# Performance work log

Measured on AMD Instinct MI355X. Metric: run time of the kernel, lower is better.

Reference implementation:

```python
import jax, jax.numpy as jnp
import numpy as np

N = 50000   # nodes
D = 128     # hidden dim
E_NS = 250000  # non-self-loop edges
B = 4096    # sessions
NEG_SLOPE = 0.01  # F.leaky_relu default


def setup_inputs() -> dict:
    key = jax.random.key(0)
    ks = jax.random.split(key, 8)
    x = jax.random.normal(ks[0], (N, D), jnp.float32)
    src = jax.random.randint(ks[1], (E_NS,), 0, N)
    off = jax.random.randint(ks[2], (E_NS,), 1, N)
    dst = (src + off) % N  # guarantees src != dst
    loops = jnp.arange(N)
    edge_index = jnp.stack([jnp.concatenate([src, loops]),
                            jnp.concatenate([dst, loops])])  # [2, E_NS+N]
    batch = jnp.sort(jax.random.randint(ks[3], (N,), 0, B))
    local_sess_avg = jax.random.normal(ks[4], (B, D), jnp.float32)
    stdv = 1.0 / np.sqrt(D)
    W_alpha = jax.random.uniform(ks[5], (1, D), jnp.float32, -stdv, stdv)
    W_forward = jax.random.uniform(ks[6], (1, D), jnp.float32, -stdv, stdv)
    W_backward = jax.random.uniform(ks[7], (1, D), jnp.float32, -stdv, stdv)
    mt_sess_masks = jnp.ones((N,), jnp.int32)
    return {"x": x, "W_alpha": W_alpha, "W_forward": W_forward,
            "W_backward": W_backward, "local_sess_avg": local_sess_avg,
            "edge_index": edge_index, "batch": batch,
            "mt_sess_masks": mt_sess_masks, "n_nonself": E_NS}


def reference(x, W_alpha, W_forward, W_backward, local_sess_avg,
              edge_index, batch, mt_sess_masks, n_nonself):
    n = x.shape[0]
    src, dst = edge_index[0], edge_index[1]
    # non-self-loop edges occupy the first n_nonself columns (static int)
    src_ns, dst_ns = src[:n_nonself], dst[:n_nonself]
    # expanded edges = original edges + reversed non-self-loop edges
    exp_src = jnp.concatenate([src, dst_ns])  # [Et]
    exp_dst = jnp.concatenate([dst, src_ns])  # [Et]

    lrelu = lambda v: jax.nn.leaky_relu(v, NEG_SLOPE)

    exp_xi = x[exp_dst]                     # [Et, D]
    exp_xj = x[exp_src]                     # [Et, D]
    alpha_query = local_sess_avg[batch[exp_dst]]  # [Et, D]
    alpha = lrelu((exp_xi * alpha_query) @ W_alpha.T)        # [Et, 1]
    beta = lrelu((x[dst] * x[src]) @ W_forward.T)            # [E, 1]
    rbeta = lrelu((x[dst_ns] * x[src_ns]) @ W_backward.T)    # [E_ns, 1]
    logits = (jnp.concatenate([beta, rbeta], axis=0) + alpha)[:, 0]  # [Et]

    # segment softmax over target nodes (every node has a self-loop)
    seg_max = jax.lax.stop_gradient(
        jax.ops.segment_max(logits, exp_dst, num_segments=n))
    ex = jnp.exp(logits - seg_max[exp_dst])
    denom = jax.ops.segment_sum(ex, exp_dst, num_segments=n)
    aij = ex / denom[exp_dst]

    # scatter-add weighted neighbor features
    aggr = jax.ops.segment_sum(aij[:, None] * exp_xj, exp_dst, num_segments=n)

    # update: masked nodes take aggregate, others keep x; residual add
    new_x = jnp.where((mt_sess_masks == 1)[:, None], aggr, x)
    return new_x + x
```

## Files before the change

### kernel.cpp

```cpp
#include <hip/hip_runtime.h>

#define NEG_SLOPE 0.01f

__device__ __forceinline__ float lrelu(float v) { return v > 0.f ? v : NEG_SLOPE * v; }

__device__ __forceinline__ float dot4(float4 a, float4 b) {
    return a.x * b.x + a.y * b.y + a.z * b.z + a.w * b.w;
}


__global__ void count_kernel(const int* __restrict__ EI0, const int* __restrict__ EI1,
                             int* __restrict__ counts, int E_total, int E_NS) {
    int t = blockIdx.x * blockDim.x + threadIdx.x;
    int n1v = E_total >> 2, n0v = E_NS >> 2;
    if (t < n1v) {
        int4 d = ((const int4*)EI1)[t];
        atomicAdd(&counts[d.x], 1); atomicAdd(&counts[d.y], 1);
        atomicAdd(&counts[d.z], 1); atomicAdd(&counts[d.w], 1);
    } else if (t < n1v + n0v) {
        int4 d = ((const int4*)EI0)[t - n1v];
        atomicAdd(&counts[d.x], 1); atomicAdd(&counts[d.y], 1);
        atomicAdd(&counts[d.z], 1); atomicAdd(&counts[d.w], 1);
    } else if (t == n1v + n0v) {
        for (int e = E_total & ~3; e < E_total; e++) atomicAdd(&counts[EI1[e]], 1);
        for (int e = E_NS & ~3; e < E_NS; e++) atomicAdd(&counts[EI0[e]], 1);
    }
}

__global__ void scan1_kernel(const int* __restrict__ counts, int* __restrict__ rowptrL,
                             int* __restrict__ blockSums, int N) {
    __shared__ int tmp[256];
    int tid = threadIdx.x;
    int gid = blockIdx.x * 256 + tid;
    int v = (gid < N) ? counts[gid] : 0;
    tmp[tid] = v;
    __syncthreads();
#pragma unroll
    for (int off = 1; off < 256; off <<= 1) {
        int t = (tid >= off) ? tmp[tid - off] : 0;
        __syncthreads();
        tmp[tid] += t;
        __syncthreads();
    }
    if (gid < N) rowptrL[gid] = tmp[tid] - v;
    if (tid == 255) blockSums[blockIdx.x] = tmp[255];
}

__global__ void scan2_kernel(int* __restrict__ blockSums, int nb) {
    __shared__ int tmp[256];
    int tid = threadIdx.x;
    int v = (tid < nb) ? blockSums[tid] : 0;
    tmp[tid] = v;
    __syncthreads();
#pragma unroll
    for (int off = 1; off < 256; off <<= 1) {
        int t = (tid >= off) ? tmp[tid - off] : 0;
        __syncthreads();
        tmp[tid] += t;
        __syncthreads();
    }
    if (tid < nb) blockSums[tid] = tmp[tid] - v;
}

__device__ __forceinline__ void placeEdge(int s, int d, unsigned flag,
                                          const int* __restrict__ rowptrL,
                                          const int* __restrict__ blockSums,
                                          int* __restrict__ cursor, int* __restrict__ csr) {
    int pos = atomicAdd(&cursor[d], 1);
    csr[rowptrL[d] + blockSums[d >> 8] + pos] = (int)((unsigned)s | flag);
}

__global__ void fill_kernel(const int* __restrict__ EI0, const int* __restrict__ EI1,
                            const int* __restrict__ rowptrL, const int* __restrict__ blockSums,
                            int* __restrict__ cursor, int* __restrict__ csr,
                            int E_total, int E_NS) {
    int t = blockIdx.x * blockDim.x + threadIdx.x;
    int n1v = E_total >> 2, n0v = E_NS >> 2;
    if (t < n1v) {
        int4 s = ((const int4*)EI0)[t];
        int4 d = ((const int4*)EI1)[t];
        placeEdge(s.x, d.x, 0u, rowptrL, blockSums, cursor, csr);
        placeEdge(s.y, d.y, 0u, rowptrL, blockSums, cursor, csr);
        placeEdge(s.z, d.z, 0u, rowptrL, blockSums, cursor, csr);
        placeEdge(s.w, d.w, 0u, rowptrL, blockSums, cursor, csr);
    } else if (t < n1v + n0v) {
        int u = t - n1v;
        int4 s = ((const int4*)EI1)[u];
        int4 d = ((const int4*)EI0)[u];
        placeEdge(s.x, d.x, 0x80000000u, rowptrL, blockSums, cursor, csr);
        placeEdge(s.y, d.y, 0x80000000u, rowptrL, blockSums, cursor, csr);
        placeEdge(s.z, d.z, 0x80000000u, rowptrL, blockSums, cursor, csr);
        placeEdge(s.w, d.w, 0x80000000u, rowptrL, blockSums, cursor, csr);
    } else if (t == n1v + n0v) {
        for (int e = E_total & ~3; e < E_total; e++)
            placeEdge(EI0[e], EI1[e], 0u, rowptrL, blockSums, cursor, csr);
        for (int e = E_NS & ~3; e < E_NS; e++)
            placeEdge(EI1[e], EI0[e], 0x80000000u, rowptrL, blockSums, cursor, csr);
    }
}

__global__ void gather_kernel(const float4* __restrict__ x4,
                              const float4* __restrict__ Wf4, const float4* __restrict__ Wb4,
                              const int* __restrict__ rowptrL, const int* __restrict__ blockSums,
                              const int* __restrict__ counts, const int* __restrict__ csr,
                              const int* __restrict__ mask,
                              float4* __restrict__ out4, int N) {
    int tid = blockIdx.x * blockDim.x + threadIdx.x;
    int node = tid >> 4;
    int sub = threadIdx.x & 15;
    bool active = (node < N);
    int nodeSafe = active ? node : 0;

    long long base = (long long)nodeSafe * 32;
    float4 xda = x4[base + sub];
    float4 xdb = x4[base + 16 + sub];
    float4 wfa = Wf4[sub], wfb = Wf4[16 + sub];
    float4 wba = Wb4[sub], wbb = Wb4[16 + sub];
    float4 yfa = {xda.x * wfa.x, xda.y * wfa.y, xda.z * wfa.z, xda.w * wfa.w};
    float4 yfb = {xdb.x * wfb.x, xdb.y * wfb.y, xdb.z * wfb.z, xdb.w * wfb.w};
    float4 yba = {xda.x * wba.x, xda.y * wba.y, xda.z * wba.z, xda.w * wba.w};
    float4 ybb = {xdb.x * wbb.x, xdb.y * wbb.y, xdb.z * wbb.z, xdb.w * wbb.w};

    int cnt = active ? counts[node] : 0;
    int beg = active ? (rowptrL[node] + blockSums[node >> 8]) : 0;

    int cm = cnt;
    cm = max(cm, __shfl_xor(cm, 16, 64));
    cm = max(cm, __shfl_xor(cm, 32, 64));

    float m = -INFINITY, l = 0.f;
    float4 Oa = {0.f, 0.f, 0.f, 0.f}, Ob = {0.f, 0.f, 0.f, 0.f};

    for (int i = 0; i < cm; i += 2) {
        bool v0 = (i < cnt), v1 = (i + 1 < cnt);
        int e0 = v0 ? csr[beg + i] : 0;
        int e1 = v1 ? csr[beg + i + 1] : 0;
        long long s0 = (long long)(e0 & 0x7fffffff) * 32;
        long long s1 = (long long)(e1 & 0x7fffffff) * 32;
        float4 r0a = x4[s0 + sub], r0b = x4[s0 + 16 + sub];
        float4 r1a = x4[s1 + sub], r1b = x4[s1 + 16 + sub];
        bool f0 = (e0 < 0), f1 = (e1 < 0);

        float p0 = dot4(r0a, f0 ? yba : yfa) + dot4(r0b, f0 ? ybb : yfb);
        float p1 = dot4(r1a, f1 ? yba : yfa) + dot4(r1b, f1 ? ybb : yfb);
#pragma unroll
        for (int sh = 1; sh < 16; sh <<= 1) {
            p0 += __shfl_xor(p0, sh, 64);
            p1 += __shfl_xor(p1, sh, 64);
        }

        if (v0) {
            float lg = lrelu(p0);
            float mn = fmaxf(m, lg);
            float sc = __expf(m - mn), ev = __expf(lg - mn);
            l = l * sc + ev;
            Oa.x = Oa.x * sc + ev * r0a.x; Oa.y = Oa.y * sc + ev * r0a.y;
            Oa.z = Oa.z * sc + ev * r0a.z; Oa.w = Oa.w * sc + ev * r0a.w;
            Ob.x = Ob.x * sc + ev * r0b.x; Ob.y = Ob.y * sc + ev * r0b.y;
            Ob.z = Ob.z * sc + ev * r0b.z; Ob.w = Ob.w * sc + ev * r0b.w;
            m = mn;
        }
        if (v1) {
            float lg = lrelu(p1);
            float mn = fmaxf(m, lg);
            float sc = __expf(m - mn), ev = __expf(lg - mn);
            l = l * sc + ev;
            Oa.x = Oa.x * sc + ev * r1a.x; Oa.y = Oa.y * sc + ev * r1a.y;
            Oa.z = Oa.z * sc + ev * r1a.z; Oa.w = Oa.w * sc + ev * r1a.w;
            Ob.x = Ob.x * sc + ev * r1b.x; Ob.y = Ob.y * sc + ev * r1b.y;
            Ob.z = Ob.z * sc + ev * r1b.z; Ob.w = Ob.w * sc + ev * r1b.w;
            m = mn;
        }
    }

    if (active) {
        float inv = (l > 0.f) ? 1.f / l : 0.f;
        float4 ra, rb;
        if (mask[node] == 1) {
            ra = {Oa.x * inv + xda.x, Oa.y * inv + xda.y, Oa.z * inv + xda.z, Oa.w * inv + xda.w};
            rb = {Ob.x * inv + xdb.x, Ob.y * inv + xdb.y, Ob.z * inv + xdb.z, Ob.w * inv + xdb.w};
        } else {
            ra = {2.f * xda.x, 2.f * xda.y, 2.f * xda.z, 2.f * xda.w};
            rb = {2.f * xdb.x, 2.f * xdb.y, 2.f * xdb.z, 2.f * xdb.w};
        }
        out4[base + sub] = ra;
        out4[base + 16 + sub] = rb;
    }
}

extern "C" void kernel_launch(void* const* d_in, const int* in_sizes, int n_in,
                              void* d_out, int out_size, void* d_ws, size_t ws_size,
                              hipStream_t stream) {
    const float* x   = (const float*)d_in[0];
    const float* Wf  = (const float*)d_in[2];
    const float* Wb  = (const float*)d_in[3];
    const int* EI    = (const int*)d_in[5];
    const int* mask  = (const int*)d_in[7];

    int N = in_sizes[6];
    int E_total = in_sizes[5] / 2;
    int E_NS = E_total - N;
    int EE = E_total + E_NS;

    const int* EI0 = EI;
    const int* EI1 = EI + E_total;

    char* ws = (char*)d_ws;
    int* counts    = (int*)ws;
    int* cursor    = (int*)(ws + (size_t)N * 4);
    int* rowptrL   = (int*)(ws + (size_t)2 * N * 4);
    int* blockSums = (int*)(ws + (size_t)3 * N * 4);
    int* csr       = (int*)(ws + (size_t)3 * N * 4 + 1024);

    hipMemsetAsync(counts, 0, (size_t)2 * N * 4, stream);

    const int BLK = 256;
    int edgeVecThreads = (E_total >> 2) + (E_NS >> 2) + 1;
    int edgeVecBlocks = (edgeVecThreads + BLK - 1) / BLK;
    int scanBlocks = (N + BLK - 1) / BLK;
    int nodeBlocks = (N + 15) / 16;

    count_kernel<<<edgeVecBlocks, BLK, 0, stream>>>(EI0, EI1, counts, E_total, E_NS);
    scan1_kernel<<<scanBlocks, BLK, 0, stream>>>(counts, rowptrL, blockSums, N);
    scan2_kernel<<<1, BLK, 0, stream>>>(blockSums, scanBlocks);
    fill_kernel<<<edgeVecBlocks, BLK, 0, stream>>>(EI0, EI1, rowptrL, blockSums, cursor, csr,
                                                   E_total, E_NS);
    gather_kernel<<<nodeBlocks, BLK, 0, stream>>>(
        (const float4*)x, (const float4*)Wf, (const float4*)Wb,
        rowptrL, blockSums, counts, csr, mask, (float4*)d_out, N);
}
```

Before: 184.9 us.

## Fuse CSR build into one cooperative kernel with grid syncs; prefetch CSR indices

Replaces the memset and the four separate count, scan and fill launches with a single cooperative kernel of 512 blocks that uses grid-wide syncs between phases. This removes launch gaps and the memset. The gather kernel now prefetches the next pair of CSR entries one iteration ahead and skips edge traversal for unmasked nodes. The trade-offs are grid-sync latency and the loss of int4-vectorised edge loads in the grid-stride loops.

```diff
diff --git a/kernel.cpp b/kernel.cpp
--- a/kernel.cpp
+++ b/kernel.cpp
@@ -1,4 +1,7 @@
 #include <hip/hip_runtime.h>
+#include <hip/hip_cooperative_groups.h>
+
+namespace cg = cooperative_groups;
 
 #define NEG_SLOPE 0.01f
 
@@ -8,94 +11,64 @@
     return a.x * b.x + a.y * b.y + a.z * b.z + a.w * b.w;
 }
 
-
-__global__ void count_kernel(const int* __restrict__ EI0, const int* __restrict__ EI1,
-                             int* __restrict__ counts, int E_total, int E_NS) {
-    int t = blockIdx.x * blockDim.x + threadIdx.x;
-    int n1v = E_total >> 2, n0v = E_NS >> 2;
-    if (t < n1v) {
-        int4 d = ((const int4*)EI1)[t];
-        atomicAdd(&counts[d.x], 1); atomicAdd(&counts[d.y], 1);
-        atomicAdd(&counts[d.z], 1); atomicAdd(&counts[d.w], 1);
-    } else if (t < n1v + n0v) {
-        int4 d = ((const int4*)EI0)[t - n1v];
-        atomicAdd(&counts[d.x], 1); atomicAdd(&counts[d.y], 1);
-        atomicAdd(&counts[d.z], 1); atomicAdd(&counts[d.w], 1);
-    } else if (t == n1v + n0v) {
-        for (int e = E_total & ~3; e < E_total; e++) atomicAdd(&counts[EI1[e]], 1);
-        for (int e = E_NS & ~3; e < E_NS; e++) atomicAdd(&counts[EI0[e]], 1);
-    }
-}
-
-__global__ void scan1_kernel(const int* __restrict__ counts, int* __restrict__ rowptrL,
-                             int* __restrict__ blockSums, int N) {
+__global__ void build_csr_coop(const int* __restrict__ EI0, const int* __restrict__ EI1,
+                               int* __restrict__ counts, int* __restrict__ cursor,
+                               int* __restrict__ rowptrL, int* __restrict__ blockSums,
+                               int* __restrict__ csr, int E_total, int E_NS, int N) {
+    cg::grid_group grid = cg::this_grid();
     __shared__ int tmp[256];
-    int tid = threadIdx.x;
-    int gid = blockIdx.x * 256 + tid;
-    int v = (gid < N) ? counts[gid] : 0;
-    tmp[tid] = v;
-    __syncthreads();
+    int tid = blockIdx.x * blockDim.x + threadIdx.x;
+    int nth = gridDim.x * blockDim.x;
+    int EE = E_total + E_NS;
+
+    for (int i = tid; i < N; i += nth) { counts[i] = 0; cursor[i] = 0; }
+    grid.sync();
+
+    for (int e = tid; e < EE; e += nth) {
+        int d = (e < E_total) ? EI1[e] : EI0[e - E_total];
+        atomicAdd(&counts[d], 1);
+    }
+    grid.sync();
+
+    int nChunks = (N + 255) / 256;
+    if (blockIdx.x < nChunks) {
+        int gid = blockIdx.x * 256 + threadIdx.x;
+        int v = (gid < N) ? counts[gid] : 0;
+        tmp[threadIdx.x] = v;
+        __syncthreads();
 #pragma unroll
-    for (int off = 1; off < 256; off <<= 1) {
-        int t = (tid >= off) ? tmp[tid - off] : 0;
+        for (int off = 1; off < 256; off <<= 1) {
+            int t = (threadIdx.x >= off) ? tmp[threadIdx.x - off] : 0;
+            __syncthreads();
+            tmp[threadIdx.x] += t;
+            __syncthreads();
+        }
+        if (gid < N) rowptrL[gid] = tmp[threadIdx.x] - v;
+        if (threadIdx.x == 255) blockSums[blockIdx.x] = tmp[255];
+    }
+    grid.sync();
+
+    if (blockIdx.x == 0) {
+        int v = (threadIdx.x < nChunks) ? blockSums[threadIdx.x] : 0;
+        tmp[threadIdx.x] = v;
         __syncthreads();
-        tmp[tid] += t;
-        __syncthreads();
-    }
-    if (gid < N) rowptrL[gid] = tmp[tid] - v;
-    if (tid == 255) blockSums[blockIdx.x] = tmp[255];
-}
-
-__global__ void scan2_kernel(int* __restrict__ blockSums, int nb) {
-    __shared__ int tmp[256];
-    int tid = threadIdx.x;
-    int v = (tid < nb) ? blockSums[tid] : 0;
-    tmp[tid] = v;
-    __syncthreads();
 #pragma unroll
-    for (int off = 1; off < 256; off <<= 1) {
-        int t = (tid >= off) ? tmp[tid - off] : 0;
-        __syncthreads();
-        tmp[tid] += t;
-        __syncthreads();
-    }
-    if (tid < nb) blockSums[tid] = tmp[tid] - v;
-}
-
-__device__ __forceinline__ void placeEdge(int s, int d, unsigned flag,
-                                          const int* __restrict__ rowptrL,
-                                          const int* __restrict__ blockSums,
-                                          int* __restrict__ cursor, int* __restrict__ csr) {
-    int pos = atomicAdd(&cursor[d], 1);
-    csr[rowptrL[d] + blockSums[d >> 8] + pos] = (int)((unsigned)s | flag);
-}
-
-__global__ void fill_kernel(const int* __restrict__ EI0, const int* __restrict__ EI1,
-                            const int* __restrict__ rowptrL, const int* __restrict__ blockSums,
-                            int* __restrict__ cursor, int* __restrict__ csr,
-                            int E_total, int E_NS) {
-    int t = blockIdx.x * blockDim.x + threadIdx.x;
-    int n1v = E_total >> 2, n0v = E_NS >> 2;
-    if (t < n1v) {
-        int4 s = ((const int4*)EI0)[t];
-        int4 d = ((const int4*)EI1)[t];
-        placeEdge(s.x, d.x, 0u, rowptrL, blockSums, cursor, csr);
-        placeEdge(s.y, d.y, 0u, rowptrL, blockSums, cursor, csr);
-        placeEdge(s.z, d.z, 0u, rowptrL, blockSums, cursor, csr);
-        placeEdge(s.w, d.w, 0u, rowptrL, blockSums, cursor, csr);
-    } else if (t < n1v + n0v) {
-        int u = t - n1v;
-        int4 s = ((const int4*)EI1)[u];
-        int4 d = ((const int4*)EI0)[u];
-        placeEdge(s.x, d.x, 0x80000000u, rowptrL, blockSums, cursor, csr);
-        placeEdge(s.y, d.y, 0x80000000u, rowptrL, blockSums, cursor, csr);
-        placeEdge(s.z, d.z, 0x80000000u, rowptrL, blockSums, cursor, csr);
-        placeEdge(s.w, d.w, 0x80000000u, rowptrL, blockSums, cursor, csr);
-    } else if (t == n1v + n0v) {
-        for (int e = E_total & ~3; e < E_total; e++)
-            placeEdge(EI0[e], EI1[e], 0u, rowptrL, blockSums, cursor, csr);
-        for (int e = E_NS & ~3; e < E_NS; e++)
-            placeEdge(EI1[e], EI0[e], 0x80000000u, rowptrL, blockSums, cursor, csr);
+        for (int off = 1; off < 256; off <<= 1) {
+            int t = (threadIdx.x >= off) ? tmp[threadIdx.x - off] : 0;
+            __syncthreads();
+            tmp[threadIdx.x] += t;
+            __syncthreads();
+        }
+        if (threadIdx.x < nChunks) blockSums[threadIdx.x] = tmp[threadIdx.x] - v;
+    }
+    grid.sync();
+
+    for (int e = tid; e < EE; e += nth) {
+        int s, d; unsigned flag;
+        if (e < E_total) { s = EI0[e]; d = EI1[e]; flag = 0u; }
+        else { int e2 = e - E_total; s = EI1[e2]; d = EI0[e2]; flag = 0x80000000u; }
+        int pos = atomicAdd(&cursor[d], 1);
+        csr[rowptrL[d] + blockSums[d >> 8] + pos] = (int)((unsigned)s | flag);
     }
 }
 
@@ -114,6 +87,10 @@
     long long base = (long long)nodeSafe * 32;
     float4 xda = x4[base + sub];
     float4 xdb = x4[base + 16 + sub];
+    int msk = active ? mask[nodeSafe] : 0;
+    int cnt = (active && msk == 1) ? counts[nodeSafe] : 0;
+    int beg = active ? (rowptrL[nodeSafe] + blockSums[nodeSafe >> 8]) : 0;
+
     float4 wfa = Wf4[sub], wfb = Wf4[16 + sub];
     float4 wba = Wb4[sub], wbb = Wb4[16 + sub];
     float4 yfa = {xda.x * wfa.x, xda.y * wfa.y, xda.z * wfa.z, xda.w * wfa.w};
@@ -121,9 +98,6 @@
     float4 yba = {xda.x * wba.x, xda.y * wba.y, xda.z * wba.z, xda.w * wba.w};
     float4 ybb = {xdb.x * wbb.x, xdb.y * wbb.y, xdb.z * wbb.z, xdb.w * wbb.w};
 
-    int cnt = active ? counts[node] : 0;
-    int beg = active ? (rowptrL[node] + blockSums[node >> 8]) : 0;
-
     int cm = cnt;
     cm = max(cm, __shfl_xor(cm, 16, 64));
     cm = max(cm, __shfl_xor(cm, 32, 64));
@@ -131,10 +105,15 @@
     float m = -INFINITY, l = 0.f;
     float4 Oa = {0.f, 0.f, 0.f, 0.f}, Ob = {0.f, 0.f, 0.f, 0.f};
 
+    int cur0 = (cnt > 0) ? csr[beg] : 0;
+    int cur1 = (cnt > 1) ? csr[beg + 1] : 0;
+
     for (int i = 0; i < cm; i += 2) {
         bool v0 = (i < cnt), v1 = (i + 1 < cnt);
-        int e0 = v0 ? csr[beg + i] : 0;
-        int e1 = v1 ? csr[beg + i + 1] : 0;
+        int e0 = cur0, e1 = cur1;
+        cur0 = (i + 2 < cnt) ? csr[beg + i + 2] : 0;
+        cur1 = (i + 3 < cnt) ? csr[beg + i + 3] : 0;
+
         long long s0 = (long long)(e0 & 0x7fffffff) * 32;
         long long s1 = (long long)(e1 & 0x7fffffff) * 32;
         float4 r0a = x4[s0 + sub], r0b = x4[s0 + 16 + sub];
@@ -174,9 +153,9 @@
     }
 
     if (active) {
-        float inv = (l > 0.f) ? 1.f / l : 0.f;
         float4 ra, rb;
-        if (mask[node] == 1) {
+        if (msk == 1) {
+            float inv = (l > 0.f) ? 1.f / l : 0.f;
             ra = {Oa.x * inv + xda.x, Oa.y * inv + xda.y, Oa.z * inv + xda.z, Oa.w * inv + xda.w};
             rb = {Ob.x * inv + xdb.x, Ob.y * inv + xdb.y, Ob.z * inv + xdb.z, Ob.w * inv + xdb.w};
         } else {
@@ -200,7 +179,6 @@
     int N = in_sizes[6];
     int E_total = in_sizes[5] / 2;
     int E_NS = E_total - N;
-    int EE = E_total + E_NS;
 
     const int* EI0 = EI;
     const int* EI1 = EI + E_total;
@@ -212,20 +190,16 @@
     int* blockSums = (int*)(ws + (size_t)3 * N * 4);
     int* csr       = (int*)(ws + (size_t)3 * N * 4 + 1024);
 
-    hipMemsetAsync(counts, 0, (size_t)2 * N * 4, stream);
-
-    const int BLK = 256;
-    int edgeVecThreads = (E_total >> 2) + (E_NS >> 2) + 1;
-    int edgeVecBlocks = (edgeVecThreads + BLK - 1) / BLK;
-    int scanBlocks = (N + BLK - 1) / BLK;
+    {
+        void* args[] = {(void*)&EI0, (void*)&EI1, (void*)&counts, (void*)&cursor,
+                        (void*)&rowptrL, (void*)&blockSums, (void*)&csr,
+                        (void*)&E_total, (void*)&E_NS, (void*)&N};
+        hipLaunchCooperativeKernel((void*)build_csr_coop, dim3(512), dim3(256),
+                                   args, 0, stream);
+    }
+
     int nodeBlocks = (N + 15) / 16;
-
-    count_kernel<<<edgeVecBlocks, BLK, 0, stream>>>(EI0, EI1, counts, E_total, E_NS);
-    scan1_kernel<<<scanBlocks, BLK, 0, stream>>>(counts, rowptrL, blockSums, N);
-    scan2_kernel<<<1, BLK, 0, stream>>>(blockSums, scanBlocks);
-    fill_kernel<<<edgeVecBlocks, BLK, 0, stream>>>(EI0, EI1, rowptrL, blockSums, cursor, csr,
-                                                   E_total, E_NS);
-    gather_kernel<<<nodeBlocks, BLK, 0, stream>>>(
+    gather_kernel<<<nodeBlocks, 256, 0, stream>>>(
         (const float4*)x, (const float4*)Wf, (const float4*)Wb,
         rowptrL, blockSums, counts, csr, mask, (float4*)d_out, N);
 }
```

Measured after the change: 387.7 us. 2.1x slower.
